# Optimization experiments

Hardware: AMD Instinct MI355X
Metric: run time of the kernel (lower is better)

## Reference

```python
import jax, jax.numpy as jnp
import numpy as np

DIM_M = 512
NEG_INF = -1e30


def setup_inputs() -> dict:
    key = jax.random.key(0)
    k1, k2, k3, k4, k5, k6, k7 = jax.random.split(key, 7)
    B, Lc, Lq, d = 16, 1024, 512, DIM_M
    C = jax.random.normal(k1, (B, Lc, d), dtype=jnp.float32)
    Q = jax.random.normal(k2, (B, Lq, d), dtype=jnp.float32)
    cmask = jax.random.randint(k3, (B, Lc), 0, 2).astype(jnp.float32)
    qmask = jax.random.randint(k4, (B, Lq), 0, 2).astype(jnp.float32)
    lim = np.sqrt(1.0 / d)
    w = jax.random.uniform(k5, (3 * d,), minval=-lim, maxval=lim, dtype=jnp.float32)
    # out_linear: Linear(4d -> d), torch default init
    bound = np.sqrt(1.0 / (4 * d))
    out_w = jax.random.uniform(k6, (d, 4 * d), minval=-bound, maxval=bound, dtype=jnp.float32)
    out_b = jax.random.uniform(k7, (d,), minval=-bound, maxval=bound, dtype=jnp.float32)
    return {"C": C, "Q": Q, "cmask": cmask, "qmask": qmask, "w": w, "out_w": out_w, "out_b": out_b}


def _mask_logits(t, m):
    return t * m + (1.0 - m) * NEG_INF


def reference(C, Q, cmask, qmask, w, out_w, out_b):
    d = C.shape[-1]
    w1, w2, w3 = w[:d], w[d:2 * d], w[2 * d:]
    # Decomposed trilinear similarity (same math as cat([Ct,Qt,Ct*Qt]) @ w):
    # S[b,i,j] = C[b,i]@w1 + Q[b,j]@w2 + (C[b,i]*w3) @ Q[b,j]
    S = (C @ w1)[:, :, None] + (Q @ w2)[:, None, :] \
        + jnp.einsum('bid,bjd->bij', C * w3, Q)  # [B, Lc, Lq]
    qm = qmask[:, None, :]  # [B, 1, Lq]
    cm = cmask[:, :, None]  # [B, Lc, 1]
    S1 = jax.nn.softmax(_mask_logits(S, qm), axis=2)  # over Lq
    S2 = jax.nn.softmax(_mask_logits(S, cm), axis=1)  # over Lc
    A = jnp.einsum('bij,bjd->bid', S1, Q)  # [B, Lc, d]
    # bmm(bmm(S1, S2^T), C) == S1 @ (S2^T @ C) by associativity (cheaper)
    S2TC = jnp.einsum('bij,bid->bjd', S2, C)  # [B, Lq, d]
    Bm = jnp.einsum('bij,bjd->bid', S1, S2TC)  # [B, Lc, d]
    out = jnp.concatenate([C, A, C * A, C * Bm], axis=2)  # [B, Lc, 4d]
    # dropout inactive (inference); out_linear
    return out @ out_w.T + out_b
```

## Files before the change

kernel.cpp:

```cpp
#include <hip/hip_runtime.h>
#include <hip/hip_bf16.h>


#define NB 16
#define LC 1024
#define LQ 512
#define DM 512
#define D4 2048
#define NEGINF (-1e30f)

typedef __bf16 v8bf __attribute__((ext_vector_type(8)));
typedef __bf16 v4bf __attribute__((ext_vector_type(4)));
typedef float  v4f  __attribute__((ext_vector_type(4)));

#define MFMA16 __builtin_amdgcn_mfma_f32_16x16x32_bf16

#define GLOAD16(gp, lp) __builtin_amdgcn_global_load_lds( \
    (const __attribute__((address_space(1))) void*)(gp), \
    (__attribute__((address_space(3))) void*)(lp), 16, 0, 0)

#define GEMM_PROLOG \
  __shared__ __bf16 Al[2][128 * 32], Bl[2][128 * 32]; \
  int bx = blockIdx.x, by = blockIdx.y, bz = blockIdx.z; \
  xcd_remap(bx, by, bz); \
  const int b = bz, i0 = by * 128, n0 = bx * 128; \
  const int t = threadIdx.x, lane = t & 63, wave = t >> 6; \
  const int wm = wave >> 1, wn = wave & 1, quad = lane >> 4, col = lane & 15; \
  const int srow = wave * 32 + (lane >> 2), scol = (lane & 3) * 8; \
  v4f acc[4][4]; \
  _Pragma("unroll") for (int x = 0; x < 4; ++x) \
  _Pragma("unroll") for (int y = 0; y < 4; ++y) \
  _Pragma("unroll") for (int r = 0; r < 4; ++r) acc[x][y][r] = 0.f;

#define GEMM_STAGE(buf, Aptr, Bptr, LDGA, LDGB, k0) \
  do { _Pragma("unroll") for (int u = 0; u < 2; ++u) { \
    GLOAD16((Aptr) + (size_t)(u * 16) * (LDGA) + (k0), &Al[buf][(wave * 32 + u * 16) * 32]); \
    GLOAD16((Bptr) + (size_t)(u * 16) * (LDGB) + (k0), &Bl[buf][(wave * 32 + u * 16) * 32]); \
  } } while (0)

#define GEMM_COMPUTE(buf) \
  do { \
    v8bf af_[4], bf_[4]; \
    _Pragma("unroll") for (int x = 0; x < 4; ++x) \
      af_[x] = *(const v8bf*)&Al[buf][(wm * 64 + x * 16 + col) * 32 + quad * 8]; \
    _Pragma("unroll") for (int y = 0; y < 4; ++y) \
      bf_[y] = *(const v8bf*)&Bl[buf][(wn * 64 + y * 16 + col) * 32 + quad * 8]; \
    _Pragma("unroll") for (int x = 0; x < 4; ++x) \
    _Pragma("unroll") for (int y = 0; y < 4; ++y) \
      acc[x][y] = MFMA16(af_[x], bf_[y], acc[x][y], 0, 0, 0); \
  } while (0)

#define GEMM_SYNC() \
  do { asm volatile("s_waitcnt vmcnt(0)" ::: "memory"); \
       __builtin_amdgcn_s_barrier(); } while (0)

#define GEMM_KLOOP(Arow, Brow, LDGA, LDGB, KEXT) \
  { GEMM_STAGE(0, Arow, Brow, LDGA, LDGB, 0); \
    GEMM_SYNC(); \
    int cur_ = 0; \
    for (int k0 = 0; k0 < (KEXT); k0 += 32) { \
      const int kn_ = k0 + 32; \
      if (kn_ < (KEXT)) GEMM_STAGE(cur_ ^ 1, Arow, Brow, LDGA, LDGB, kn_); \
      GEMM_COMPUTE(cur_); \
      GEMM_SYNC(); \
      cur_ ^= 1; \
    } }

__device__ __forceinline__ void xcd_remap(int& bx, int& by, int& bz) {
  const int gx = gridDim.x, gy = gridDim.y, gz = gridDim.z;
  int flat = bx + gx * (by + gy * bz);
  int per = (gx * gy * gz) >> 3;
  int nw = (flat & 7) * per + (flat >> 3);
  bx = nw % gx;
  int r = nw / gx;
  by = r % gy;
  bz = r / gy;
}

__global__ void k_rowdots(const float* __restrict__ C, const float* __restrict__ Q,
                          const float* __restrict__ w,
                          float* __restrict__ cw1, float* __restrict__ qw2,
                          __bf16* __restrict__ Cbf, __bf16* __restrict__ Qw3) {
  const int wid = threadIdx.x >> 6, lane = threadIdx.x & 63;
  const int row = blockIdx.x * 4 + wid;
  const bool isC = row < NB * LC;
  const int lr = isC ? row : row - NB * LC;
  const float* src = (isC ? C : Q) + (size_t)lr * DM;
  const float* wv  = isC ? w : (w + DM);
  const float* w3  = w + 2 * DM;
  __bf16* dst = (isC ? Cbf : Qw3) + (size_t)lr * DM;
  float v = 0.f;
#pragma unroll
  for (int s = 0; s < 2; ++s) {
    const int k = lane * 4 + s * 256;
    float4 f = *(const float4*)(src + k);
    float4 g = *(const float4*)(wv + k);
    v += f.x * g.x + f.y * g.y + f.z * g.z + f.w * g.w;
    v4bf h;
    if (isC) {
      h[0] = (__bf16)f.x; h[1] = (__bf16)f.y; h[2] = (__bf16)f.z; h[3] = (__bf16)f.w;
    } else {
      float4 s3 = *(const float4*)(w3 + k);
      h[0] = (__bf16)(f.x * s3.x); h[1] = (__bf16)(f.y * s3.y);
      h[2] = (__bf16)(f.z * s3.z); h[3] = (__bf16)(f.w * s3.w);
    }
    *(v4bf*)(dst + k) = h;
  }
#pragma unroll
  for (int off = 32; off; off >>= 1) v += __shfl_down(v, off, 64);
  if (lane == 0) {
    if (isC) cw1[row] = v;
    else     qw2[lr] = v;
  }
}

__device__ __forceinline__ void transpose_tile(const float* __restrict__ in,
                                               __bf16* __restrict__ outT,
                                               int R, int Cd, int tbx, int tby, int tb) {
  __shared__ __bf16 tile[64][66];
  const int r0 = tby * 64, c0 = tbx * 64;
  const int tr = threadIdx.x >> 6, tc = threadIdx.x & 63;
  const float* inb = in + (size_t)tb * R * Cd;
  __bf16* outb = outT + (size_t)tb * Cd * R;
  for (int r = tr; r < 64; r += 4)
    tile[r][tc] = (__bf16)inb[(size_t)(r0 + r) * Cd + c0 + tc];
  __syncthreads();
  for (int c = tr; c < 64; c += 4)
    outb[(size_t)(c0 + c) * R + r0 + tc] = tile[tc][c];
}

__global__ void k_prep(const float* __restrict__ C, const float* __restrict__ Q,
                       const float* __restrict__ OW,
                       __bf16* __restrict__ CT, __bf16* __restrict__ QT,
                       __bf16* __restrict__ OWb) {
  const int id = blockIdx.x;
  if (id < 2048) {
    transpose_tile(C, CT, LC, DM, id & 7, (id >> 3) & 15, id >> 7);
  } else if (id < 3072) {
    const int id2 = id - 2048;
    transpose_tile(Q, QT, LQ, DM, id2 & 7, (id2 >> 3) & 7, id2 >> 6);
  } else {
    const size_t i = ((size_t)(id - 3072) * 256 + threadIdx.x) * 4;
    float4 f = *(const float4*)(OW + i);
    v4bf h; h[0] = (__bf16)f.x; h[1] = (__bf16)f.y; h[2] = (__bf16)f.z; h[3] = (__bf16)f.w;
    *(v4bf*)(OWb + i) = h;
  }
}

__global__ void k_cvt2(const float* __restrict__ Cf, const float* __restrict__ OW,
                       __bf16* __restrict__ Cb3, __bf16* __restrict__ OWb) {
  const size_t NC = (size_t)NB * LC * DM;
  size_t i = ((size_t)blockIdx.x * 256 + threadIdx.x) * 4;
  const float* src; __bf16* dst; size_t j;
  if (i < NC) { src = Cf; dst = Cb3; j = i; }
  else        { src = OW; dst = OWb; j = i - NC; }
  float4 f = *(const float4*)(src + j);
  v4bf h; h[0] = (__bf16)f.x; h[1] = (__bf16)f.y; h[2] = (__bf16)f.z; h[3] = (__bf16)f.w;
  *(v4bf*)(OWb ? dst : dst + j - j) = h;
}

__global__ void k_cvt2b(const float* __restrict__ Cf, const float* __restrict__ OW,
                        __bf16* __restrict__ Cb3, __bf16* __restrict__ OWb) {
  const size_t NC = (size_t)NB * LC * DM;
  size_t i = ((size_t)blockIdx.x * 256 + threadIdx.x) * 4;
  if (i < NC) {
    float4 f = *(const float4*)(Cf + i);
    v4bf h; h[0] = (__bf16)f.x; h[1] = (__bf16)f.y; h[2] = (__bf16)f.z; h[3] = (__bf16)f.w;
    *(v4bf*)(Cb3 + i) = h;
  } else {
    size_t j = i - NC;
    float4 f = *(const float4*)(OW + j);
    v4bf h; h[0] = (__bf16)f.x; h[1] = (__bf16)f.y; h[2] = (__bf16)f.z; h[3] = (__bf16)f.w;
    *(v4bf*)(OWb + j) = h;
  }
}

__global__ __launch_bounds__(256) void k_mfma_S(
    const __bf16* __restrict__ Cbf, const __bf16* __restrict__ Qw3,
    const float* __restrict__ cw1, const float* __restrict__ qw2,
    float* __restrict__ S) {
  GEMM_PROLOG
  const __bf16* Arow = Cbf + (size_t)b * LC * DM + (size_t)(i0 + srow) * DM + scol;
  const __bf16* Brow = Qw3 + (size_t)b * LQ * DM + (size_t)(n0 + srow) * DM + scol;
  GEMM_KLOOP(Arow, Brow, DM, DM, DM)
  float* Sb = S + (size_t)b * LC * LQ;
#pragma unroll
  for (int x = 0; x < 4; ++x) {
    const int mB = i0 + wm * 64 + x * 16 + quad * 4;
    float cv[4];
#pragma unroll
    for (int r = 0; r < 4; ++r) cv[r] = cw1[b * LC + mB + r];
#pragma unroll
    for (int y = 0; y < 4; ++y) {
      const int j = n0 + wn * 64 + y * 16 + col;
      const float qv = qw2[b * LQ + j];
#pragma unroll
      for (int r = 0; r < 4; ++r)
        Sb[(size_t)(mB + r) * LQ + j] = acc[x][y][r] + cv[r] + qv;
    }
  }
}

__global__ __launch_bounds__(1024) void k_softstat(
    const float* __restrict__ S, const float* __restrict__ qmask,
    const float* __restrict__ cmask, __bf16* __restrict__ S1,
    float2* __restrict__ pstat) {
  __shared__ float2 cst[16][LQ];
  const int b = blockIdx.y, ic = blockIdx.x;
  const int tid = threadIdx.x, wv = tid >> 6, lane = tid & 63;
  const float* qm  = qmask + b * LQ;
  const float* cm  = cmask + b * LC + ic * 64;
  const float* Sb  = S  + ((size_t)b * LC + ic * 64) * LQ;
  __bf16*      S1b = S1 + ((size_t)b * LC + ic * 64) * LQ;
  float colm[8], cols[8];
#pragma unroll
  for (int tt = 0; tt < 8; ++tt) { colm[tt] = -3e38f; cols[tt] = 0.f; }
  for (int it = 0; it < 4; ++it) {
    const int r = wv * 4 + it;
    const float cmv = cm[r];
    const float* Srow = Sb + (size_t)r * LQ;
    float sv[8], l1[8];
    float m = -3e38f;
#pragma unroll
    for (int tt = 0; tt < 8; ++tt) {
      int j = lane + 64 * tt;
      sv[tt] = Srow[j];
      float qv = qm[j];
      l1[tt] = qv * sv[tt] + (1.f - qv) * NEGINF;
      m = fmaxf(m, l1[tt]);
    }
#pragma unroll
    for (int off = 32; off; off >>= 1) m = fmaxf(m, __shfl_xor(m, off, 64));
    float e[8], s = 0.f;
#pragma unroll
    for (int tt = 0; tt < 8; ++tt) { e[tt] = __expf(l1[tt] - m); s += e[tt]; }
#pragma unroll
    for (int off = 32; off; off >>= 1) s += __shfl_xor(s, off, 64);
    const float inv = 1.f / s;
#pragma unroll
    for (int tt = 0; tt < 8; ++tt)
      S1b[(size_t)r * LQ + lane + 64 * tt] = (__bf16)(e[tt] * inv);
    if (cmv != 0.f) {
#pragma unroll
      for (int tt = 0; tt < 8; ++tt) {
        float l2 = sv[tt];
        if (l2 > colm[tt]) { cols[tt] *= __expf(colm[tt] - l2); colm[tt] = l2; }
        cols[tt] += __expf(l2 - colm[tt]);
      }
    }
  }
#pragma unroll
  for (int tt = 0; tt < 8; ++tt) cst[wv][lane + 64 * tt] = make_float2(colm[tt], cols[tt]);
  __syncthreads();
  if (tid < LQ) {
    float M = -3e38f, Sd = 0.f;
#pragma unroll
    for (int k = 0; k < 16; ++k) {
      float2 p = cst[k][tid];
      float nM = fmaxf(M, p.x);
      Sd = Sd * __expf(M - nM) + p.y * __expf(p.x - nM);
      M = nM;
    }
    pstat[((size_t)(b * 16 + ic) * LQ) + tid] = make_float2(M, Sd);
  }
}

__global__ void k_colwrite(const float* __restrict__ S, const float* __restrict__ cmask,
                           const float2* __restrict__ pstat, __bf16* __restrict__ S2T) {
  __shared__ float Mf[64], If[64];
  __shared__ __bf16 tile[64][66];
  const int b = blockIdx.z, ic = blockIdx.y, j0 = blockIdx.x * 64;
  const int c = threadIdx.x & 63, ip = threadIdx.x >> 6;
  if (threadIdx.x < 64) {
    float M = -3e38f, Sd = 0.f;
#pragma unroll
    for (int k = 0; k < 16; ++k) {
      float2 p = pstat[((size_t)(b * 16 + k) * LQ) + j0 + threadIdx.x];
      float nM = fmaxf(M, p.x);
      Sd = Sd * __expf(M - nM) + p.y * __expf(p.x - nM);
      M = nM;
    }
    Mf[threadIdx.x] = M; If[threadIdx.x] = 1.f / Sd;
  }
  __syncthreads();
  const float M = Mf[c], inv = If[c];
  const float* Sb = S + ((size_t)b * LC + ic * 64) * LQ;
  const float* cm = cmask + b * LC + ic * 64;
  for (int r = ip; r < 64; r += 4) {
    if (cm[r] != 0.f)
      tile[r][c] = (__bf16)(__expf(Sb[(size_t)r * LQ + j0 + c] - M) * inv);
    else
      tile[r][c] = (__bf16)0.f;
  }
  __syncthreads();
  __bf16* S2Tb = S2T + ((size_t)b * LQ + j0) * LC + ic * 64;
  for (int jr = ip; jr < 64; jr += 4)
    S2Tb[(size_t)jr * LC + c] = tile[c][jr];
}

__global__ __launch_bounds__(256) void k_mfma_A(
    const __bf16* __restrict__ S1, const __bf16* __restrict__ QT,
    const float* __restrict__ Cf, __bf16* __restrict__ Aw, __bf16* __restrict__ CAw) {
  GEMM_PROLOG
  const __bf16* Arow = S1 + (size_t)b * LC * LQ + (size_t)(i0 + srow) * LQ + scol;
  const __bf16* Brow = QT + (size_t)b * DM * LQ + (size_t)(n0 + srow) * LQ + scol;
  GEMM_KLOOP(Arow, Brow, LQ, LQ, LQ)
  const float* Cb = Cf + (size_t)b * LC * DM;
  __bf16* Ab  = Aw  + (size_t)b * LC * DM;
  __bf16* CAb = CAw + (size_t)b * LC * DM;
#pragma unroll
  for (int x = 0; x < 4; ++x) {
    const int mB = i0 + wm * 64 + x * 16 + quad * 4;
#pragma unroll
    for (int y = 0; y < 4; ++y) {
      const int n = n0 + wn * 64 + y * 16 + col;
#pragma unroll
      for (int r = 0; r < 4; ++r) {
        const float av = acc[x][y][r];
        const float cv = Cb[(size_t)(mB + r) * DM + n];
        Ab[(size_t)(mB + r) * DM + n]  = (__bf16)av;
        CAb[(size_t)(mB + r) * DM + n] = (__bf16)(av * cv);
      }
    }
  }
}

__global__ __launch_bounds__(256) void k_mfma_T(
    const __bf16* __restrict__ S2T, const __bf16* __restrict__ CT, __bf16* __restrict__ S2TCT) {
  GEMM_PROLOG
  const int j0 = i0;
  const __bf16* Arow = S2T + (size_t)b * LQ * LC + (size_t)(j0 + srow) * LC + scol;
  const __bf16* Brow = CT  + (size_t)b * DM * LC + (size_t)(n0 + srow) * LC + scol;
  GEMM_KLOOP(Arow, Brow, LC, LC, LC)
#pragma unroll
  for (int x = 0; x < 4; ++x) {
    const int jB = j0 + wm * 64 + x * 16 + quad * 4;
#pragma unroll
    for (int y = 0; y < 4; ++y) {
      const int n = n0 + wn * 64 + y * 16 + col;
      v4bf h;
#pragma unroll
      for (int r = 0; r < 4; ++r) h[r] = (__bf16)acc[x][y][r];
      *(v4bf*)&S2TCT[((size_t)b * DM + n) * LQ + jB] = h;
    }
  }
}

__global__ __launch_bounds__(256) void k_mfma_Bm(
    const __bf16* __restrict__ S1, const __bf16* __restrict__ S2TCT,
    const float* __restrict__ Cf, __bf16* __restrict__ CBw) {
  GEMM_PROLOG
  const __bf16* Arow = S1    + (size_t)b * LC * LQ + (size_t)(i0 + srow) * LQ + scol;
  const __bf16* Brow = S2TCT + (size_t)b * DM * LQ + (size_t)(n0 + srow) * LQ + scol;
  GEMM_KLOOP(Arow, Brow, LQ, LQ, LQ)
  const float* Cb = Cf + (size_t)b * LC * DM;
  __bf16* CBb = CBw + (size_t)b * LC * DM;
#pragma unroll
  for (int x = 0; x < 4; ++x) {
    const int mB = i0 + wm * 64 + x * 16 + quad * 4;
#pragma unroll
    for (int y = 0; y < 4; ++y) {
      const int n = n0 + wn * 64 + y * 16 + col;
#pragma unroll
      for (int r = 0; r < 4; ++r) {
        const float cv = Cb[(size_t)(mB + r) * DM + n];
        CBb[(size_t)(mB + r) * DM + n] = (__bf16)(acc[x][y][r] * cv);
      }
    }
  }
}

__global__ __launch_bounds__(256) void k_mfma_out(
    const __bf16* __restrict__ Cb3, const __bf16* __restrict__ Aw,
    const __bf16* __restrict__ CAw, const __bf16* __restrict__ CBw,
    const __bf16* __restrict__ OWb, const float* __restrict__ ob,
    float* __restrict__ out) {
  GEMM_PROLOG
  const size_t rowoff = (size_t)b * LC * DM + (size_t)(i0 + srow) * DM + scol;
  const __bf16* As0 = Cb3 + rowoff;
  const __bf16* As1 = Aw  + rowoff;
  const __bf16* As2 = CAw + rowoff;
  const __bf16* As3 = CBw + rowoff;
  const __bf16* Brow0 = OWb + (size_t)(n0 + srow) * D4 + scol;
  GEMM_STAGE(0, As0, Brow0, DM, D4, 0);
  GEMM_SYNC();
  int cur_ = 0;
#pragma unroll
  for (int seg = 0; seg < 4; ++seg) {
    const __bf16* Arow  = (seg == 0) ? As0 : (seg == 1) ? As1 : (seg == 2) ? As2 : As3;
    const __bf16* Anext = (seg == 0) ? As1 : (seg == 1) ? As2 : As3;
    const __bf16* Brow  = Brow0 + seg * DM;
    const __bf16* Bnext = Brow0 + (seg < 3 ? seg + 1 : 3) * DM;
    for (int k0 = 0; k0 < DM; k0 += 32) {
      const int kn_ = k0 + 32;
      if (kn_ < DM)      GEMM_STAGE(cur_ ^ 1, Arow, Brow, DM, D4, kn_);
      else if (seg < 3)  GEMM_STAGE(cur_ ^ 1, Anext, Bnext, DM, D4, 0);
      GEMM_COMPUTE(cur_);
      GEMM_SYNC();
      cur_ ^= 1;
    }
  }
  float* outb = out + (size_t)b * LC * DM;
#pragma unroll
  for (int x = 0; x < 4; ++x) {
    const int mB = i0 + wm * 64 + x * 16 + quad * 4;
#pragma unroll
    for (int y = 0; y < 4; ++y) {
      const int n = n0 + wn * 64 + y * 16 + col;
      const float bv = ob[n];
#pragma unroll
      for (int r = 0; r < 4; ++r)
        outb[(size_t)(mB + r) * DM + n] = acc[x][y][r] + bv;
    }
  }
}

extern "C" void kernel_launch(void* const* d_in, const int* in_sizes, int n_in,
                              void* d_out, int out_size, void* d_ws, size_t ws_size,
                              hipStream_t stream) {
  const float* C     = (const float*)d_in[0];
  const float* Q     = (const float*)d_in[1];
  const float* cmask = (const float*)d_in[2];
  const float* qmask = (const float*)d_in[3];
  const float* w     = (const float*)d_in[4];
  const float* out_w = (const float*)d_in[5];
  const float* out_b = (const float*)d_in[6];
  float* out = (float*)d_out;

  char* base = (char*)d_ws;
  float*  cw1   = (float*)base;
  float*  qw2   = (float*)(base + 65536);
  char*   R     = base + 131072;
  float*  S     = (float*)R;
  __bf16* CT    = (__bf16*)R;
  __bf16* Aw    = (__bf16*)R;
  __bf16* QT    = (__bf16*)(R + (16u << 20));
  __bf16* CBw   = (__bf16*)(R + (16u << 20));
  __bf16* S1    = (__bf16*)(R + (32u << 20));
  __bf16* Qw3   = (__bf16*)(R + (48u << 20));
  __bf16* S2T   = (__bf16*)(R + (48u << 20));
  __bf16* CAw   = (__bf16*)(R + (48u << 20));
  float2* pstat = (float2*)(R + (64u << 20));
  __bf16* S2TCT = (__bf16*)(R + (64u << 20));
  (void)in_sizes; (void)n_in; (void)out_size;

  const size_t need_big = 131072 + (90ull << 20);
  const bool bigws = ws_size >= need_big;

  __bf16 *Cbf, *Cbf3, *OWbf;
  if (bigws) {
    Cbf  = (__bf16*)(R + (72u << 20));
    Cbf3 = Cbf;
    OWbf = (__bf16*)(R + (88u << 20));
  } else {
    Cbf  = (__bf16*)(R + (32u << 20));
    Cbf3 = (__bf16*)(R + (32u << 20));
    OWbf = (__bf16*)(R + (64u << 20));
  }

  k_rowdots<<<(NB * LC + NB * LQ) / 4, 256, 0, stream>>>(C, Q, w, cw1, qw2, Cbf, Qw3);
  k_mfma_S<<<dim3(LQ / 128, LC / 128, NB), 256, 0, stream>>>(Cbf, Qw3, cw1, qw2, S);
  k_softstat<<<dim3(LC / 64, NB), 1024, 0, stream>>>(S, qmask, cmask, S1, pstat);
  k_colwrite<<<dim3(LQ / 64, LC / 64, NB), 256, 0, stream>>>(S, cmask, pstat, S2T);
  k_prep<<<bigws ? 4096 : 3072, 256, 0, stream>>>(C, Q, out_w, CT, QT, OWbf);
  k_mfma_T<<<dim3(DM / 128, LQ / 128, NB), 256, 0, stream>>>(S2T, CT, S2TCT);
  k_mfma_A<<<dim3(DM / 128, LC / 128, NB), 256, 0, stream>>>(S1, QT, C, Aw, CAw);
  k_mfma_Bm<<<dim3(DM / 128, LC / 128, NB), 256, 0, stream>>>(S1, S2TCT, C, CBw);
  if (!bigws)
    k_cvt2b<<<(NB * LC * DM + DM * D4) / 1024, 256, 0, stream>>>(C, out_w, Cbf3, OWbf);
  k_mfma_out<<<dim3(DM / 128, LC / 128, NB), 256, 0, stream>>>(Cbf3, Aw, CAw, CBw, OWbf, out_b, out);
}
```

Before: 285.2 us.

## Retile GEMMs to 128x64 with K=64 stages and XOR-swizzled LDS

All MFMA GEMM kernels move from 128x128 tiles with K-step 32 to 128x64 tiles with K-step 64. The LDS layout gains an XOR swizzle on 16-byte chunks to avoid bank conflicts, and grids double in the N dimension. Separately, the C transpose in k_prep reads the existing bf16 copy instead of fp32 when the big workspace is available. The aim is higher occupancy, fewer barriers per K, and conflict-free LDS reads, at the cost of lower per-block reuse (the B tile is half as wide) and more redundant A-tile loads.

```diff
diff --git a/kernel.cpp b/kernel.cpp
--- a/kernel.cpp
+++ b/kernel.cpp
@@ -20,33 +20,46 @@
     (__attribute__((address_space(3))) void*)(lp), 16, 0, 0)
 
 #define GEMM_PROLOG \
-  __shared__ __bf16 Al[2][128 * 32], Bl[2][128 * 32]; \
+  __shared__ __bf16 Al[2][128 * 64], Bl[2][64 * 64]; \
   int bx = blockIdx.x, by = blockIdx.y, bz = blockIdx.z; \
   xcd_remap(bx, by, bz); \
-  const int b = bz, i0 = by * 128, n0 = bx * 128; \
+  const int b = bz, i0 = by * 128, n0 = bx * 64; \
   const int t = threadIdx.x, lane = t & 63, wave = t >> 6; \
   const int wm = wave >> 1, wn = wave & 1, quad = lane >> 4, col = lane & 15; \
-  const int srow = wave * 32 + (lane >> 2), scol = (lane & 3) * 8; \
-  v4f acc[4][4]; \
+  const int srA = wave * 32 + (lane >> 3); \
+  const int srB = wave * 16 + (lane >> 3); \
+  const int swz = ((lane & 7) ^ (lane >> 3)) * 8; \
+  const int q80 = ((quad ^ (col & 7)) * 8); \
+  const int q81 = (((4 + quad) ^ (col & 7)) * 8); \
+  v4f acc[4][2]; \
   _Pragma("unroll") for (int x = 0; x < 4; ++x) \
-  _Pragma("unroll") for (int y = 0; y < 4; ++y) \
+  _Pragma("unroll") for (int y = 0; y < 2; ++y) \
   _Pragma("unroll") for (int r = 0; r < 4; ++r) acc[x][y][r] = 0.f;
 
 #define GEMM_STAGE(buf, Aptr, Bptr, LDGA, LDGB, k0) \
-  do { _Pragma("unroll") for (int u = 0; u < 2; ++u) { \
-    GLOAD16((Aptr) + (size_t)(u * 16) * (LDGA) + (k0), &Al[buf][(wave * 32 + u * 16) * 32]); \
-    GLOAD16((Bptr) + (size_t)(u * 16) * (LDGB) + (k0), &Bl[buf][(wave * 32 + u * 16) * 32]); \
-  } } while (0)
+  do { \
+    _Pragma("unroll") for (int u = 0; u < 4; ++u) \
+      GLOAD16((Aptr) + (size_t)(u * 8) * (LDGA) + (k0), &Al[buf][(wave * 32 + u * 8) * 64]); \
+    _Pragma("unroll") for (int u = 0; u < 2; ++u) \
+      GLOAD16((Bptr) + (size_t)(u * 8) * (LDGB) + (k0), &Bl[buf][(wave * 16 + u * 8) * 64]); \
+  } while (0)
 
 #define GEMM_COMPUTE(buf) \
   do { \
-    v8bf af_[4], bf_[4]; \
+    v8bf af_[4], bf_[2]; \
     _Pragma("unroll") for (int x = 0; x < 4; ++x) \
-      af_[x] = *(const v8bf*)&Al[buf][(wm * 64 + x * 16 + col) * 32 + quad * 8]; \
-    _Pragma("unroll") for (int y = 0; y < 4; ++y) \
-      bf_[y] = *(const v8bf*)&Bl[buf][(wn * 64 + y * 16 + col) * 32 + quad * 8]; \
+      af_[x] = *(const v8bf*)&Al[buf][(wm * 64 + x * 16 + col) * 64 + q80]; \
+    _Pragma("unroll") for (int y = 0; y < 2; ++y) \
+      bf_[y] = *(const v8bf*)&Bl[buf][(wn * 32 + y * 16 + col) * 64 + q80]; \
     _Pragma("unroll") for (int x = 0; x < 4; ++x) \
-    _Pragma("unroll") for (int y = 0; y < 4; ++y) \
+    _Pragma("unroll") for (int y = 0; y < 2; ++y) \
+      acc[x][y] = MFMA16(af_[x], bf_[y], acc[x][y], 0, 0, 0); \
+    _Pragma("unroll") for (int x = 0; x < 4; ++x) \
+      af_[x] = *(const v8bf*)&Al[buf][(wm * 64 + x * 16 + col) * 64 + q81]; \
+    _Pragma("unroll") for (int y = 0; y < 2; ++y) \
+      bf_[y] = *(const v8bf*)&Bl[buf][(wn * 32 + y * 16 + col) * 64 + q81]; \
+    _Pragma("unroll") for (int x = 0; x < 4; ++x) \
+    _Pragma("unroll") for (int y = 0; y < 2; ++y) \
       acc[x][y] = MFMA16(af_[x], bf_[y], acc[x][y], 0, 0, 0); \
   } while (0)
 
@@ -58,8 +71,8 @@
   { GEMM_STAGE(0, Arow, Brow, LDGA, LDGB, 0); \
     GEMM_SYNC(); \
     int cur_ = 0; \
-    for (int k0 = 0; k0 < (KEXT); k0 += 32) { \
-      const int kn_ = k0 + 32; \
+    for (int k0 = 0; k0 < (KEXT); k0 += 64) { \
+      const int kn_ = k0 + 64; \
       if (kn_ < (KEXT)) GEMM_STAGE(cur_ ^ 1, Arow, Brow, LDGA, LDGB, kn_); \
       GEMM_COMPUTE(cur_); \
       GEMM_SYNC(); \
@@ -114,9 +127,9 @@
   }
 }
 
-__device__ __forceinline__ void transpose_tile(const float* __restrict__ in,
-                                               __bf16* __restrict__ outT,
-                                               int R, int Cd, int tbx, int tby, int tb) {
+__device__ __forceinline__ void transpose_tile_f32(const float* __restrict__ in,
+                                                   __bf16* __restrict__ outT,
+                                                   int R, int Cd, int tbx, int tby, int tb) {
   __shared__ __bf16 tile[64][66];
   const int r0 = tby * 64, c0 = tbx * 64;
   const int tr = threadIdx.x >> 6, tc = threadIdx.x & 63;
@@ -129,34 +142,38 @@
     outb[(size_t)(c0 + c) * R + r0 + tc] = tile[tc][c];
 }
 
-__global__ void k_prep(const float* __restrict__ C, const float* __restrict__ Q,
-                       const float* __restrict__ OW,
+__device__ __forceinline__ void transpose_tile_bf(const __bf16* __restrict__ in,
+                                                  __bf16* __restrict__ outT,
+                                                  int R, int Cd, int tbx, int tby, int tb) {
+  __shared__ __bf16 tile[64][66];
+  const int r0 = tby * 64, c0 = tbx * 64;
+  const int tr = threadIdx.x >> 6, tc = threadIdx.x & 63;
+  const __bf16* inb = in + (size_t)tb * R * Cd;
+  __bf16* outb = outT + (size_t)tb * Cd * R;
+  for (int r = tr; r < 64; r += 4)
+    tile[r][tc] = inb[(size_t)(r0 + r) * Cd + c0 + tc];
+  __syncthreads();
+  for (int c = tr; c < 64; c += 4)
+    outb[(size_t)(c0 + c) * R + r0 + tc] = tile[tc][c];
+}
+
+__global__ void k_prep(const float* __restrict__ C, const __bf16* __restrict__ Cbf,
+                       const float* __restrict__ Q, const float* __restrict__ OW,
                        __bf16* __restrict__ CT, __bf16* __restrict__ QT,
-                       __bf16* __restrict__ OWb) {
+                       __bf16* __restrict__ OWb, int use_cbf) {
   const int id = blockIdx.x;
   if (id < 2048) {
-    transpose_tile(C, CT, LC, DM, id & 7, (id >> 3) & 15, id >> 7);
+    if (use_cbf) transpose_tile_bf(Cbf, CT, LC, DM, id & 7, (id >> 3) & 15, id >> 7);
+    else         transpose_tile_f32(C,  CT, LC, DM, id & 7, (id >> 3) & 15, id >> 7);
   } else if (id < 3072) {
     const int id2 = id - 2048;
-    transpose_tile(Q, QT, LQ, DM, id2 & 7, (id2 >> 3) & 7, id2 >> 6);
+    transpose_tile_f32(Q, QT, LQ, DM, id2 & 7, (id2 >> 3) & 7, id2 >> 6);
   } else {
     const size_t i = ((size_t)(id - 3072) * 256 + threadIdx.x) * 4;
     float4 f = *(const float4*)(OW + i);
     v4bf h; h[0] = (__bf16)f.x; h[1] = (__bf16)f.y; h[2] = (__bf16)f.z; h[3] = (__bf16)f.w;
     *(v4bf*)(OWb + i) = h;
   }
-}
-
-__global__ void k_cvt2(const float* __restrict__ Cf, const float* __restrict__ OW,
-                       __bf16* __restrict__ Cb3, __bf16* __restrict__ OWb) {
-  const size_t NC = (size_t)NB * LC * DM;
-  size_t i = ((size_t)blockIdx.x * 256 + threadIdx.x) * 4;
-  const float* src; __bf16* dst; size_t j;
-  if (i < NC) { src = Cf; dst = Cb3; j = i; }
-  else        { src = OW; dst = OWb; j = i - NC; }
-  float4 f = *(const float4*)(src + j);
-  v4bf h; h[0] = (__bf16)f.x; h[1] = (__bf16)f.y; h[2] = (__bf16)f.z; h[3] = (__bf16)f.w;
-  *(v4bf*)(OWb ? dst : dst + j - j) = h;
 }
 
 __global__ void k_cvt2b(const float* __restrict__ Cf, const float* __restrict__ OW,
@@ -180,8 +197,8 @@
     const float* __restrict__ cw1, const float* __restrict__ qw2,
     float* __restrict__ S) {
   GEMM_PROLOG
-  const __bf16* Arow = Cbf + (size_t)b * LC * DM + (size_t)(i0 + srow) * DM + scol;
-  const __bf16* Brow = Qw3 + (size_t)b * LQ * DM + (size_t)(n0 + srow) * DM + scol;
+  const __bf16* Arow = Cbf + (size_t)b * LC * DM + (size_t)(i0 + srA) * DM + swz;
+  const __bf16* Brow = Qw3 + (size_t)b * LQ * DM + (size_t)(n0 + srB) * DM + swz;
   GEMM_KLOOP(Arow, Brow, DM, DM, DM)
   float* Sb = S + (size_t)b * LC * LQ;
 #pragma unroll
@@ -191,8 +208,8 @@
 #pragma unroll
     for (int r = 0; r < 4; ++r) cv[r] = cw1[b * LC + mB + r];
 #pragma unroll
-    for (int y = 0; y < 4; ++y) {
-      const int j = n0 + wn * 64 + y * 16 + col;
+    for (int y = 0; y < 2; ++y) {
+      const int j = n0 + wn * 32 + y * 16 + col;
       const float qv = qw2[b * LQ + j];
 #pragma unroll
       for (int r = 0; r < 4; ++r)
@@ -302,8 +319,8 @@
     const __bf16* __restrict__ S1, const __bf16* __restrict__ QT,
     const float* __restrict__ Cf, __bf16* __restrict__ Aw, __bf16* __restrict__ CAw) {
   GEMM_PROLOG
-  const __bf16* Arow = S1 + (size_t)b * LC * LQ + (size_t)(i0 + srow) * LQ + scol;
-  const __bf16* Brow = QT + (size_t)b * DM * LQ + (size_t)(n0 + srow) * LQ + scol;
+  const __bf16* Arow = S1 + (size_t)b * LC * LQ + (size_t)(i0 + srA) * LQ + swz;
+  const __bf16* Brow = QT + (size_t)b * DM * LQ + (size_t)(n0 + srB) * LQ + swz;
   GEMM_KLOOP(Arow, Brow, LQ, LQ, LQ)
   const float* Cb = Cf + (size_t)b * LC * DM;
   __bf16* Ab  = Aw  + (size_t)b * LC * DM;
@@ -312,8 +329,8 @@
   for (int x = 0; x < 4; ++x) {
     const int mB = i0 + wm * 64 + x * 16 + quad * 4;
 #pragma unroll
-    for (int y = 0; y < 4; ++y) {
-      const int n = n0 + wn * 64 + y * 16 + col;
+    for (int y = 0; y < 2; ++y) {
+      const int n = n0 + wn * 32 + y * 16 + col;
 #pragma unroll
       for (int r = 0; r < 4; ++r) {
         const float av = acc[x][y][r];
@@ -329,15 +346,15 @@
     const __bf16* __restrict__ S2T, const __bf16* __restrict__ CT, __bf16* __restrict__ S2TCT) {
   GEMM_PROLOG
   const int j0 = i0;
-  const __bf16* Arow = S2T + (size_t)b * LQ * LC + (size_t)(j0 + srow) * LC + scol;
-  const __bf16* Brow = CT  + (size_t)b * DM * LC + (size_t)(n0 + srow) * LC + scol;
+  const __bf16* Arow = S2T + (size_t)b * LQ * LC + (size_t)(j0 + srA) * LC + swz;
+  const __bf16* Brow = CT  + (size_t)b * DM * LC + (size_t)(n0 + srB) * LC + swz;
   GEMM_KLOOP(Arow, Brow, LC, LC, LC)
 #pragma unroll
   for (int x = 0; x < 4; ++x) {
     const int jB = j0 + wm * 64 + x * 16 + quad * 4;
 #pragma unroll
-    for (int y = 0; y < 4; ++y) {
-      const int n = n0 + wn * 64 + y * 16 + col;
+    for (int y = 0; y < 2; ++y) {
+      const int n = n0 + wn * 32 + y * 16 + col;
       v4bf h;
 #pragma unroll
       for (int r = 0; r < 4; ++r) h[r] = (__bf16)acc[x][y][r];
@@ -350,8 +367,8 @@
     const __bf16* __restrict__ S1, const __bf16* __restrict__ S2TCT,
     const float* __restrict__ Cf, __bf16* __restrict__ CBw) {
   GEMM_PROLOG
-  const __bf16* Arow = S1    + (size_t)b * LC * LQ + (size_t)(i0 + srow) * LQ + scol;
-  const __bf16* Brow = S2TCT + (size_t)b * DM * LQ + (size_t)(n0 + srow) * LQ + scol;
+  const __bf16* Arow = S1    + (size_t)b * LC * LQ + (size_t)(i0 + srA) * LQ + swz;
+  const __bf16* Brow = S2TCT + (size_t)b * DM * LQ + (size_t)(n0 + srB) * LQ + swz;
   GEMM_KLOOP(Arow, Brow, LQ, LQ, LQ)
   const float* Cb = Cf + (size_t)b * LC * DM;
   __bf16* CBb = CBw + (size_t)b * LC * DM;
@@ -359,8 +376,8 @@
   for (int x = 0; x < 4; ++x) {
     const int mB = i0 + wm * 64 + x * 16 + quad * 4;
 #pragma unroll
-    for (int y = 0; y < 4; ++y) {
-      const int n = n0 + wn * 64 + y * 16 + col;
+    for (int y = 0; y < 2; ++y) {
+      const int n = n0 + wn * 32 + y * 16 + col;
 #pragma unroll
       for (int r = 0; r < 4; ++r) {
         const float cv = Cb[(size_t)(mB + r) * DM + n];
@@ -376,12 +393,12 @@
     const __bf16* __restrict__ OWb, const float* __restrict__ ob,
     float* __restrict__ out) {
   GEMM_PROLOG
-  const size_t rowoff = (size_t)b * LC * DM + (size_t)(i0 + srow) * DM + scol;
+  const size_t rowoff = (size_t)b * LC * DM + (size_t)(i0 + srA) * DM + swz;
   const __bf16* As0 = Cb3 + rowoff;
   const __bf16* As1 = Aw  + rowoff;
   const __bf16* As2 = CAw + rowoff;
   const __bf16* As3 = CBw + rowoff;
-  const __bf16* Brow0 = OWb + (size_t)(n0 + srow) * D4 + scol;
+  const __bf16* Brow0 = OWb + (size_t)(n0 + srB) * D4 + swz;
   GEMM_STAGE(0, As0, Brow0, DM, D4, 0);
   GEMM_SYNC();
   int cur_ = 0;
@@ -391,8 +408,8 @@
     const __bf16* Anext = (seg == 0) ? As1 : (seg == 1) ? As2 : As3;
     const __bf16* Brow  = Brow0 + seg * DM;
     const __bf16* Bnext = Brow0 + (seg < 3 ? seg + 1 : 3) * DM;
-    for (int k0 = 0; k0 < DM; k0 += 32) {
-      const int kn_ = k0 + 32;
+    for (int k0 = 0; k0 < DM; k0 += 64) {
+      const int kn_ = k0 + 64;
       if (kn_ < DM)      GEMM_STAGE(cur_ ^ 1, Arow, Brow, DM, D4, kn_);
       else if (seg < 3)  GEMM_STAGE(cur_ ^ 1, Anext, Bnext, DM, D4, 0);
       GEMM_COMPUTE(cur_);
@@ -405,8 +422,8 @@
   for (int x = 0; x < 4; ++x) {
     const int mB = i0 + wm * 64 + x * 16 + quad * 4;
 #pragma unroll
-    for (int y = 0; y < 4; ++y) {
-      const int n = n0 + wn * 64 + y * 16 + col;
+    for (int y = 0; y < 2; ++y) {
+      const int n = n0 + wn * 32 + y * 16 + col;
       const float bv = ob[n];
 #pragma unroll
       for (int r = 0; r < 4; ++r)
@@ -459,14 +476,15 @@
   }
 
   k_rowdots<<<(NB * LC + NB * LQ) / 4, 256, 0, stream>>>(C, Q, w, cw1, qw2, Cbf, Qw3);
-  k_mfma_S<<<dim3(LQ / 128, LC / 128, NB), 256, 0, stream>>>(Cbf, Qw3, cw1, qw2, S);
+  k_mfma_S<<<dim3(LQ / 64, LC / 128, NB), 256, 0, stream>>>(Cbf, Qw3, cw1, qw2, S);
   k_softstat<<<dim3(LC / 64, NB), 1024, 0, stream>>>(S, qmask, cmask, S1, pstat);
   k_colwrite<<<dim3(LQ / 64, LC / 64, NB), 256, 0, stream>>>(S, cmask, pstat, S2T);
-  k_prep<<<bigws ? 4096 : 3072, 256, 0, stream>>>(C, Q, out_w, CT, QT, OWbf);
-  k_mfma_T<<<dim3(DM / 128, LQ / 128, NB), 256, 0, stream>>>(S2T, CT, S2TCT);
-  k_mfma_A<<<dim3(DM / 128, LC / 128, NB), 256, 0, stream>>>(S1, QT, C, Aw, CAw);
-  k_mfma_Bm<<<dim3(DM / 128, LC / 128, NB), 256, 0, stream>>>(S1, S2TCT, C, CBw);
+  k_prep<<<bigws ? 4096 : 3072, 256, 0, stream>>>(C, Cbf, Q, out_w, CT, QT, OWbf,
+                                                  bigws ? 1 : 0);
+  k_mfma_T<<<dim3(DM / 64, LQ / 128, NB), 256, 0, stream>>>(S2T, CT, S2TCT);
+  k_mfma_A<<<dim3(DM / 64, LC / 128, NB), 256, 0, stream>>>(S1, QT, C, Aw, CAw);
+  k_mfma_Bm<<<dim3(DM / 64, LC / 128, NB), 256, 0, stream>>>(S1, S2TCT, C, CBw);
   if (!bigws)
     k_cvt2b<<<(NB * LC * DM + DM * D4) / 1024, 256, 0, stream>>>(C, out_w, Cbf3, OWbf);
-  k_mfma_out<<<dim3(DM / 128, LC / 128, NB), 256, 0, stream>>>(Cbf3, Aw, CAw, CBw, OWbf, out_b, out);
-}
+  k_mfma_out<<<dim3(DM / 64, LC / 128, NB), 256, 0, stream>>>(Cbf3, Aw, CAw, CBw, OWbf, out_b, out);
+}
```

Measured after the change: 292.6 us. 1.03x slower.

## Triple-buffer GEMM LDS pipeline with XOR swizzle and bf16 C transpose

Applied to the files above, without the earlier changes.

All MFMA GEMM kernels move from a double-buffered to a triple-buffered LDS pipeline that prefetches two k-steps ahead, using a partial vmcnt wait so loads stay in flight across the barrier. The global-to-LDS columns and the fragment reads are XOR-swizzled to cut LDS bank conflicts. k_prep can now transpose C from the already converted bf16 copy instead of re-reading fp32. The cost is more LDS per block (48KB), which may lower occupancy, and more complex pipeline edge handling.

```diff
diff --git a/kernel.cpp b/kernel.cpp
--- a/kernel.cpp
+++ b/kernel.cpp
@@ -20,50 +20,68 @@
     (__attribute__((address_space(3))) void*)(lp), 16, 0, 0)
 
 #define GEMM_PROLOG \
-  __shared__ __bf16 Al[2][128 * 32], Bl[2][128 * 32]; \
+  __shared__ __bf16 Al[3][128 * 32], Bl[3][128 * 32]; \
   int bx = blockIdx.x, by = blockIdx.y, bz = blockIdx.z; \
   xcd_remap(bx, by, bz); \
   const int b = bz, i0 = by * 128, n0 = bx * 128; \
   const int t = threadIdx.x, lane = t & 63, wave = t >> 6; \
   const int wm = wave >> 1, wn = wave & 1, quad = lane >> 4, col = lane & 15; \
-  const int srow = wave * 32 + (lane >> 2), scol = (lane & 3) * 8; \
+  const int sr32 = wave * 32 + (lane >> 2); \
+  const int swz = (((lane & 3) ^ ((lane >> 2) & 3) ^ ((lane >> 4) & 3)) * 8); \
+  const int rdx = ((quad ^ (col & 3) ^ ((col >> 2) & 3)) * 8); \
   v4f acc[4][4]; \
   _Pragma("unroll") for (int x = 0; x < 4; ++x) \
   _Pragma("unroll") for (int y = 0; y < 4; ++y) \
   _Pragma("unroll") for (int r = 0; r < 4; ++r) acc[x][y][r] = 0.f;
 
 #define GEMM_STAGE(buf, Aptr, Bptr, LDGA, LDGB, k0) \
-  do { _Pragma("unroll") for (int u = 0; u < 2; ++u) { \
-    GLOAD16((Aptr) + (size_t)(u * 16) * (LDGA) + (k0), &Al[buf][(wave * 32 + u * 16) * 32]); \
-    GLOAD16((Bptr) + (size_t)(u * 16) * (LDGB) + (k0), &Bl[buf][(wave * 32 + u * 16) * 32]); \
-  } } while (0)
+  do { \
+    GLOAD16((Aptr) + (k0),                       &Al[buf][(wave * 32) * 32]); \
+    GLOAD16((Aptr) + (size_t)16 * (LDGA) + (k0), &Al[buf][(wave * 32 + 16) * 32]); \
+    GLOAD16((Bptr) + (k0),                       &Bl[buf][(wave * 32) * 32]); \
+    GLOAD16((Bptr) + (size_t)16 * (LDGB) + (k0), &Bl[buf][(wave * 32 + 16) * 32]); \
+  } while (0)
 
 #define GEMM_COMPUTE(buf) \
   do { \
     v8bf af_[4], bf_[4]; \
     _Pragma("unroll") for (int x = 0; x < 4; ++x) \
-      af_[x] = *(const v8bf*)&Al[buf][(wm * 64 + x * 16 + col) * 32 + quad * 8]; \
+      af_[x] = *(const v8bf*)&Al[buf][(wm * 64 + x * 16 + col) * 32 + rdx]; \
     _Pragma("unroll") for (int y = 0; y < 4; ++y) \
-      bf_[y] = *(const v8bf*)&Bl[buf][(wn * 64 + y * 16 + col) * 32 + quad * 8]; \
+      bf_[y] = *(const v8bf*)&Bl[buf][(wn * 64 + y * 16 + col) * 32 + rdx]; \
     _Pragma("unroll") for (int x = 0; x < 4; ++x) \
     _Pragma("unroll") for (int y = 0; y < 4; ++y) \
       acc[x][y] = MFMA16(af_[x], bf_[y], acc[x][y], 0, 0, 0); \
   } while (0)
 
-#define GEMM_SYNC() \
+#define GEMM_SYNC4() \
+  do { asm volatile("s_waitcnt vmcnt(4)" ::: "memory"); \
+       __builtin_amdgcn_s_barrier(); } while (0)
+#define GEMM_SYNC0() \
   do { asm volatile("s_waitcnt vmcnt(0)" ::: "memory"); \
        __builtin_amdgcn_s_barrier(); } while (0)
 
+#define GEMM_ROT() do { cur_ = (cur_ == 2) ? 0 : cur_ + 1; \
+                        nx2_ = (nx2_ == 2) ? 0 : nx2_ + 1; } while (0)
+
 #define GEMM_KLOOP(Arow, Brow, LDGA, LDGB, KEXT) \
   { GEMM_STAGE(0, Arow, Brow, LDGA, LDGB, 0); \
-    GEMM_SYNC(); \
-    int cur_ = 0; \
+    GEMM_STAGE(1, Arow, Brow, LDGA, LDGB, 32); \
+    GEMM_SYNC4(); \
+    int cur_ = 0, nx2_ = 2; \
     for (int k0 = 0; k0 < (KEXT); k0 += 32) { \
-      const int kn_ = k0 + 32; \
-      if (kn_ < (KEXT)) GEMM_STAGE(cur_ ^ 1, Arow, Brow, LDGA, LDGB, kn_); \
-      GEMM_COMPUTE(cur_); \
-      GEMM_SYNC(); \
-      cur_ ^= 1; \
+      const int kn_ = k0 + 64; \
+      if (kn_ < (KEXT)) { \
+        GEMM_STAGE(nx2_, Arow, Brow, LDGA, LDGB, kn_); \
+        GEMM_COMPUTE(cur_); \
+        GEMM_SYNC4(); \
+      } else if (k0 + 32 < (KEXT)) { \
+        GEMM_COMPUTE(cur_); \
+        GEMM_SYNC0(); \
+      } else { \
+        GEMM_COMPUTE(cur_); \
+      } \
+      GEMM_ROT(); \
     } }
 
 __device__ __forceinline__ void xcd_remap(int& bx, int& by, int& bz) {
@@ -114,9 +132,9 @@
   }
 }
 
-__device__ __forceinline__ void transpose_tile(const float* __restrict__ in,
-                                               __bf16* __restrict__ outT,
-                                               int R, int Cd, int tbx, int tby, int tb) {
+__device__ __forceinline__ void transpose_tile_f32(const float* __restrict__ in,
+                                                   __bf16* __restrict__ outT,
+                                                   int R, int Cd, int tbx, int tby, int tb) {
   __shared__ __bf16 tile[64][66];
   const int r0 = tby * 64, c0 = tbx * 64;
   const int tr = threadIdx.x >> 6, tc = threadIdx.x & 63;
@@ -129,34 +147,38 @@
     outb[(size_t)(c0 + c) * R + r0 + tc] = tile[tc][c];
 }
 
-__global__ void k_prep(const float* __restrict__ C, const float* __restrict__ Q,
-                       const float* __restrict__ OW,
+__device__ __forceinline__ void transpose_tile_bf(const __bf16* __restrict__ in,
+                                                  __bf16* __restrict__ outT,
+                                                  int R, int Cd, int tbx, int tby, int tb) {
+  __shared__ __bf16 tile[64][66];
+  const int r0 = tby * 64, c0 = tbx * 64;
+  const int tr = threadIdx.x >> 6, tc = threadIdx.x & 63;
+  const __bf16* inb = in + (size_t)tb * R * Cd;
+  __bf16* outb = outT + (size_t)tb * Cd * R;
+  for (int r = tr; r < 64; r += 4)
+    tile[r][tc] = inb[(size_t)(r0 + r) * Cd + c0 + tc];
+  __syncthreads();
+  for (int c = tr; c < 64; c += 4)
+    outb[(size_t)(c0 + c) * R + r0 + tc] = tile[tc][c];
+}
+
+__global__ void k_prep(const float* __restrict__ C, const __bf16* __restrict__ Cbf,
+                       const float* __restrict__ Q, const float* __restrict__ OW,
                        __bf16* __restrict__ CT, __bf16* __restrict__ QT,
-                       __bf16* __restrict__ OWb) {
+                       __bf16* __restrict__ OWb, int use_cbf) {
   const int id = blockIdx.x;
   if (id < 2048) {
-    transpose_tile(C, CT, LC, DM, id & 7, (id >> 3) & 15, id >> 7);
+    if (use_cbf) transpose_tile_bf(Cbf, CT, LC, DM, id & 7, (id >> 3) & 15, id >> 7);
+    else         transpose_tile_f32(C,  CT, LC, DM, id & 7, (id >> 3) & 15, id >> 7);
   } else if (id < 3072) {
     const int id2 = id - 2048;
-    transpose_tile(Q, QT, LQ, DM, id2 & 7, (id2 >> 3) & 7, id2 >> 6);
+    transpose_tile_f32(Q, QT, LQ, DM, id2 & 7, (id2 >> 3) & 7, id2 >> 6);
   } else {
     const size_t i = ((size_t)(id - 3072) * 256 + threadIdx.x) * 4;
     float4 f = *(const float4*)(OW + i);
     v4bf h; h[0] = (__bf16)f.x; h[1] = (__bf16)f.y; h[2] = (__bf16)f.z; h[3] = (__bf16)f.w;
     *(v4bf*)(OWb + i) = h;
   }
-}
-
-__global__ void k_cvt2(const float* __restrict__ Cf, const float* __restrict__ OW,
-                       __bf16* __restrict__ Cb3, __bf16* __restrict__ OWb) {
-  const size_t NC = (size_t)NB * LC * DM;
-  size_t i = ((size_t)blockIdx.x * 256 + threadIdx.x) * 4;
-  const float* src; __bf16* dst; size_t j;
-  if (i < NC) { src = Cf; dst = Cb3; j = i; }
-  else        { src = OW; dst = OWb; j = i - NC; }
-  float4 f = *(const float4*)(src + j);
-  v4bf h; h[0] = (__bf16)f.x; h[1] = (__bf16)f.y; h[2] = (__bf16)f.z; h[3] = (__bf16)f.w;
-  *(v4bf*)(OWb ? dst : dst + j - j) = h;
 }
 
 __global__ void k_cvt2b(const float* __restrict__ Cf, const float* __restrict__ OW,
@@ -180,8 +202,8 @@
     const float* __restrict__ cw1, const float* __restrict__ qw2,
     float* __restrict__ S) {
   GEMM_PROLOG
-  const __bf16* Arow = Cbf + (size_t)b * LC * DM + (size_t)(i0 + srow) * DM + scol;
-  const __bf16* Brow = Qw3 + (size_t)b * LQ * DM + (size_t)(n0 + srow) * DM + scol;
+  const __bf16* Arow = Cbf + (size_t)b * LC * DM + (size_t)(i0 + sr32) * DM + swz;
+  const __bf16* Brow = Qw3 + (size_t)b * LQ * DM + (size_t)(n0 + sr32) * DM + swz;
   GEMM_KLOOP(Arow, Brow, DM, DM, DM)
   float* Sb = S + (size_t)b * LC * LQ;
 #pragma unroll
@@ -302,8 +324,8 @@
     const __bf16* __restrict__ S1, const __bf16* __restrict__ QT,
     const float* __restrict__ Cf, __bf16* __restrict__ Aw, __bf16* __restrict__ CAw) {
   GEMM_PROLOG
-  const __bf16* Arow = S1 + (size_t)b * LC * LQ + (size_t)(i0 + srow) * LQ + scol;
-  const __bf16* Brow = QT + (size_t)b * DM * LQ + (size_t)(n0 + srow) * LQ + scol;
+  const __bf16* Arow = S1 + (size_t)b * LC * LQ + (size_t)(i0 + sr32) * LQ + swz;
+  const __bf16* Brow = QT + (size_t)b * DM * LQ + (size_t)(n0 + sr32) * LQ + swz;
   GEMM_KLOOP(Arow, Brow, LQ, LQ, LQ)
   const float* Cb = Cf + (size_t)b * LC * DM;
   __bf16* Ab  = Aw  + (size_t)b * LC * DM;
@@ -329,8 +351,8 @@
     const __bf16* __restrict__ S2T, const __bf16* __restrict__ CT, __bf16* __restrict__ S2TCT) {
   GEMM_PROLOG
   const int j0 = i0;
-  const __bf16* Arow = S2T + (size_t)b * LQ * LC + (size_t)(j0 + srow) * LC + scol;
-  const __bf16* Brow = CT  + (size_t)b * DM * LC + (size_t)(n0 + srow) * LC + scol;
+  const __bf16* Arow = S2T + (size_t)b * LQ * LC + (size_t)(j0 + sr32) * LC + swz;
+  const __bf16* Brow = CT  + (size_t)b * DM * LC + (size_t)(n0 + sr32) * LC + swz;
   GEMM_KLOOP(Arow, Brow, LC, LC, LC)
 #pragma unroll
   for (int x = 0; x < 4; ++x) {
@@ -350,8 +372,8 @@
     const __bf16* __restrict__ S1, const __bf16* __restrict__ S2TCT,
     const float* __restrict__ Cf, __bf16* __restrict__ CBw) {
   GEMM_PROLOG
-  const __bf16* Arow = S1    + (size_t)b * LC * LQ + (size_t)(i0 + srow) * LQ + scol;
-  const __bf16* Brow = S2TCT + (size_t)b * DM * LQ + (size_t)(n0 + srow) * LQ + scol;
+  const __bf16* Arow = S1    + (size_t)b * LC * LQ + (size_t)(i0 + sr32) * LQ + swz;
+  const __bf16* Brow = S2TCT + (size_t)b * DM * LQ + (size_t)(n0 + sr32) * LQ + swz;
   GEMM_KLOOP(Arow, Brow, LQ, LQ, LQ)
   const float* Cb = Cf + (size_t)b * LC * DM;
   __bf16* CBb = CBw + (size_t)b * LC * DM;
@@ -376,28 +398,39 @@
     const __bf16* __restrict__ OWb, const float* __restrict__ ob,
     float* __restrict__ out) {
   GEMM_PROLOG
-  const size_t rowoff = (size_t)b * LC * DM + (size_t)(i0 + srow) * DM + scol;
-  const __bf16* As0 = Cb3 + rowoff;
-  const __bf16* As1 = Aw  + rowoff;
-  const __bf16* As2 = CAw + rowoff;
-  const __bf16* As3 = CBw + rowoff;
-  const __bf16* Brow0 = OWb + (size_t)(n0 + srow) * D4 + scol;
-  GEMM_STAGE(0, As0, Brow0, DM, D4, 0);
-  GEMM_SYNC();
-  int cur_ = 0;
+  const size_t rowoff = (size_t)b * LC * DM + (size_t)(i0 + sr32) * DM + swz;
+  const __bf16* Aseg[4] = {Cb3 + rowoff, Aw + rowoff, CAw + rowoff, CBw + rowoff};
+  const __bf16* Brow0 = OWb + (size_t)(n0 + sr32) * D4 + swz;
+  GEMM_STAGE(0, Aseg[0], Brow0, DM, D4, 0);
+  GEMM_STAGE(1, Aseg[0], Brow0, DM, D4, 32);
+  GEMM_SYNC4();
+  int cur_ = 0, nx2_ = 2;
 #pragma unroll
   for (int seg = 0; seg < 4; ++seg) {
-    const __bf16* Arow  = (seg == 0) ? As0 : (seg == 1) ? As1 : (seg == 2) ? As2 : As3;
-    const __bf16* Anext = (seg == 0) ? As1 : (seg == 1) ? As2 : As3;
-    const __bf16* Brow  = Brow0 + seg * DM;
-    const __bf16* Bnext = Brow0 + (seg < 3 ? seg + 1 : 3) * DM;
-    for (int k0 = 0; k0 < DM; k0 += 32) {
-      const int kn_ = k0 + 32;
-      if (kn_ < DM)      GEMM_STAGE(cur_ ^ 1, Arow, Brow, DM, D4, kn_);
-      else if (seg < 3)  GEMM_STAGE(cur_ ^ 1, Anext, Bnext, DM, D4, 0);
+    const __bf16* Ac = Aseg[seg];
+    const __bf16* An = Aseg[seg < 3 ? seg + 1 : 3];
+    const __bf16* Bc = Brow0 + seg * DM;
+    const __bf16* Bn = Brow0 + (seg < 3 ? seg + 1 : 3) * DM;
+    for (int j = 0; j < 14; ++j) {
+      GEMM_STAGE(nx2_, Ac, Bc, DM, D4, (j + 2) * 32);
       GEMM_COMPUTE(cur_);
-      GEMM_SYNC();
-      cur_ ^= 1;
+      GEMM_SYNC4();
+      GEMM_ROT();
+    }
+    if (seg < 3) {
+      GEMM_STAGE(nx2_, An, Bn, DM, D4, 0);
+      GEMM_COMPUTE(cur_);
+      GEMM_SYNC4();
+      GEMM_ROT();
+      GEMM_STAGE(nx2_, An, Bn, DM, D4, 32);
+      GEMM_COMPUTE(cur_);
+      GEMM_SYNC4();
+      GEMM_ROT();
+    } else {
+      GEMM_COMPUTE(cur_);
+      GEMM_SYNC0();
+      GEMM_ROT();
+      GEMM_COMPUTE(cur_);
     }
   }
   float* outb = out + (size_t)b * LC * DM;
@@ -462,7 +495,8 @@
   k_mfma_S<<<dim3(LQ / 128, LC / 128, NB), 256, 0, stream>>>(Cbf, Qw3, cw1, qw2, S);
   k_softstat<<<dim3(LC / 64, NB), 1024, 0, stream>>>(S, qmask, cmask, S1, pstat);
   k_colwrite<<<dim3(LQ / 64, LC / 64, NB), 256, 0, stream>>>(S, cmask, pstat, S2T);
-  k_prep<<<bigws ? 4096 : 3072, 256, 0, stream>>>(C, Q, out_w, CT, QT, OWbf);
+  k_prep<<<bigws ? 4096 : 3072, 256, 0, stream>>>(C, Cbf, Q, out_w, CT, QT, OWbf,
+                                                  bigws ? 1 : 0);
   k_mfma_T<<<dim3(DM / 128, LQ / 128, NB), 256, 0, stream>>>(S2T, CT, S2TCT);
   k_mfma_A<<<dim3(DM / 128, LC / 128, NB), 256, 0, stream>>>(S1, QT, C, Aw, CAw);
   k_mfma_Bm<<<dim3(DM / 128, LC / 128, NB), 256, 0, stream>>>(S1, S2TCT, C, CBw);
```

Result: no change. 289.2 us (+1.4%).
